# Kernel tuning notes

Measured on AMD Instinct MI355X. Metric: run time of the kernel, lower is better.

The kernel has to match this reference:

```python
import jax, jax.numpy as jnp
import numpy as np

PI = 3.141592653589793


def _nearest_idx(g, size):
    # PyTorch grid_sample nearest, align_corners=False: unnormalize then round half up
    x = ((g + 1.0) * size - 1.0) / 2.0
    return jnp.clip(jnp.floor(x + 0.5).astype(jnp.int32), 0, size - 1)


def setup_inputs() -> dict:
    key = jax.random.key(0)
    ks = jax.random.split(key, 12)
    B, Q, H, W, C, Cf = 1, 65536, 64, 64, 256, 128
    scale = 4  # HR is 256x256
    inp = {
        'inp_img': jax.random.uniform(ks[0], (B, 3, H, W), jnp.float32),
        'coef': jax.random.normal(ks[1], (B, C, H, W), jnp.float32) * 0.5,
        'freq': jax.random.normal(ks[2], (B, Cf, H, W), jnp.float32) * 0.5,
        'coord': jax.random.uniform(ks[3], (B, Q, 2), jnp.float32, minval=-1.0, maxval=1.0),
        'cell': jnp.full((B, Q, 2), 2.0 / (H * scale), jnp.float32),
        'w_coord_fc': jax.random.normal(ks[4], (128, 2), jnp.float32) * 0.5,
        'w_phase': jax.random.normal(ks[5], (128, 2), jnp.float32) * 0.5,
        'w1': jax.random.normal(ks[6], (256, 256), jnp.float32) * (1.0 / 16.0),
        'b1': jnp.zeros((256,), jnp.float32),
        'w2': jax.random.normal(ks[7], (256, 256), jnp.float32) * (1.0 / 16.0),
        'b2': jnp.zeros((256,), jnp.float32),
        'w3': jax.random.normal(ks[8], (3, 256), jnp.float32) * (1.0 / 16.0),
        'b3': jnp.zeros((3,), jnp.float32),
    }
    return inp


def reference(inp_img, coef, freq, coord, cell, w_coord_fc, w_phase, w1, b1, w2, b2, w3, b3):
    B, C, H, W = coef.shape
    Q = coord.shape[1]
    eps = 1e-6
    rx = 1.0 / H  # 2/H/2
    ry = 1.0 / W
    # 4 local-ensemble offsets in loop order (vx,vy) in {-1,1}x{-1,1}
    offs = jnp.array([[-1.0, -1.0], [-1.0, 1.0], [1.0, -1.0], [1.0, 1.0]], jnp.float32)
    shift = offs * jnp.array([rx, ry], jnp.float32) + eps  # [4,2]
    coord_ = jnp.clip(coord[:, None, :, :] + shift[None, :, None, :], -1.0 + eps, 1.0 - eps)  # [B,4,Q,2]

    # coord channel 0 -> H axis, channel 1 -> W axis (after flip(-1) in torch)
    iy = _nearest_idx(coord_[..., 0], H)  # [B,4,Q]
    ix = _nearest_idx(coord_[..., 1], W)
    lin = iy * W + ix  # [B,4,Q]

    def gather(fmap):  # fmap [B,Cc,H,W] -> [B,4,Q,Cc]
        Cc = fmap.shape[1]
        flat = fmap.reshape(B, Cc, H * W).transpose(0, 2, 1)  # [B,HW,Cc]
        return jax.vmap(lambda f, i: f[i])(flat, lin.reshape(B, -1)).reshape(B, 4, Q, Cc)

    q_coef = gather(coef)   # [B,4,Q,256]
    q_freq = gather(freq)   # [B,4,Q,128]

    # feat_coord at nearest pixel = pixel centers from make_coord
    qc_y = -1.0 + (2.0 * iy.astype(jnp.float32) + 1.0) / H
    qc_x = -1.0 + (2.0 * ix.astype(jnp.float32) + 1.0) / W
    rel0 = (coord[:, None, :, 0] - qc_y) * H  # [B,4,Q]
    rel1 = (coord[:, None, :, 1] - qc_x) * W
    rel_coord = jnp.stack([rel0, rel1], axis=-1)  # [B,4,Q,2]
    rel_cell = cell * jnp.array([H, W], jnp.float32)  # [B,Q,2]

    q_freq = q_freq * jnp.einsum('boqd,kd->boqk', rel_coord, w_coord_fc)
    q_freq = q_freq + jnp.einsum('bqd,kd->bqk', rel_cell, w_phase)[:, None]
    q_freq = jnp.concatenate([jnp.cos(PI * q_freq), jnp.sin(PI * q_freq)], axis=-1)  # [B,4,Q,256]

    x = q_coef * q_freq
    h = jax.nn.relu(jnp.einsum('boqc,dc->boqd', x, w1) + b1)
    h = jax.nn.relu(jnp.einsum('boqc,dc->boqd', h, w2) + b2)
    preds = jnp.einsum('boqc,dc->boqd', h, w3) + b3  # [B,4,Q,3]

    area = jnp.abs(rel0 * rel1) + 1e-9  # [B,4,Q]
    tot = jnp.sum(area, axis=1, keepdims=True)
    weights = area[:, ::-1] / tot  # swap 0<->3, 1<->2
    ret = jnp.sum(preds * weights[..., None], axis=1)  # [B,Q,3]

    # bilinear grid_sample of inp_img, padding_mode='border', align_corners=False
    hi, wi = inp_img.shape[-2:]
    gy = jnp.clip(((coord[..., 0] + 1.0) * hi - 1.0) / 2.0, 0.0, hi - 1.0)
    gx = jnp.clip(((coord[..., 1] + 1.0) * wi - 1.0) / 2.0, 0.0, wi - 1.0)
    y0 = jnp.floor(gy).astype(jnp.int32); x0 = jnp.floor(gx).astype(jnp.int32)
    y1 = jnp.clip(y0 + 1, 0, hi - 1); x1 = jnp.clip(x0 + 1, 0, wi - 1)
    wy = gy - y0.astype(jnp.float32); wx = gx - x0.astype(jnp.float32)
    img_flat = inp_img.reshape(B, 3, hi * wi).transpose(0, 2, 1)  # [B,HW,3]
    g = lambda yy, xx: jax.vmap(lambda f, i: f[i])(img_flat, yy * wi + xx)  # [B,Q,3]
    samp = (g(y0, x0) * ((1 - wy) * (1 - wx))[..., None]
            + g(y0, x1) * ((1 - wy) * wx)[..., None]
            + g(y1, x0) * (wy * (1 - wx))[..., None]
            + g(y1, x1) * (wy * wx)[..., None])
    return ret + samp
```

## Files before the change

kernel.cpp:

```cpp
#include <hip/hip_runtime.h>
#include <math.h>

typedef __bf16 bf16_t;
typedef bf16_t bf16x8 __attribute__((ext_vector_type(8)));
typedef bf16_t bf16x4 __attribute__((ext_vector_type(4)));
typedef float  f32x4  __attribute__((ext_vector_type(4)));

constexpr int H = 64, W = 64, Q = 65536;
constexpr int C = 256, CF = 128;
constexpr int QPB = 32;
constexpr int PADC = 264;


__global__ void transpose_cvt_kernel(const float* __restrict__ src, bf16_t* __restrict__ dst, int Crows) {
    __shared__ float tile[32][33];
    int bx = blockIdx.x * 32;
    int by = blockIdx.y * 32;
    int tx = threadIdx.x & 31;
    int ty = threadIdx.x >> 5;
#pragma unroll
    for (int i = 0; i < 4; i++)
        tile[ty + i * 8][tx] = src[(by + ty + i * 8) * 4096 + bx + tx];
    __syncthreads();
#pragma unroll
    for (int i = 0; i < 4; i++)
        dst[(bx + ty + i * 8) * Crows + by + tx] = (bf16_t)tile[tx][ty + i * 8];
}

__global__ void cvt_w_kernel(const float* __restrict__ w1, const float* __restrict__ w2,
                             bf16_t* __restrict__ w1b, bf16_t* __restrict__ w2b) {
    int i = blockIdx.x * 256 + threadIdx.x;
    w1b[i] = (bf16_t)w1[i];
    w2b[i] = (bf16_t)w2[i];
}

__global__ void pack_tab_kernel(const float* __restrict__ wcf, const float* __restrict__ wph,
                                float4* __restrict__ wtab) {
    int k = threadIdx.x;
    float4 v;
    v.x = wcf[k * 2 + 0]; v.y = wcf[k * 2 + 1];
    v.z = wph[k * 2 + 0]; v.w = wph[k * 2 + 1];
    wtab[k] = v;
}

__global__ void cvt_w3_kernel(const float* __restrict__ w3, bf16_t* __restrict__ w3p) {
    int k = threadIdx.x;
#pragma unroll
    for (int n = 0; n < 16; n++)
        w3p[n * 256 + k] = (n < 3) ? (bf16_t)w3[n * 256 + k] : (bf16_t)0.f;
}


#define LOADB(dst, Wptr, kb)                                                                  \
    {                                                                                         \
        dst[0] = *(const bf16x8*)((Wptr) + (wv * 32 + l15) * 256 + (kb) * 32 + l16 * 8);      \
        dst[1] = *(const bf16x8*)((Wptr) + (wv * 32 + 16 + l15) * 256 + (kb) * 32 + l16 * 8); \
    }

__global__ __launch_bounds__(512, 4)
void lte_fused_kernel(const bf16_t* __restrict__ coefT,
                      const bf16_t* __restrict__ freqT,
                      const bf16_t* __restrict__ w1b,
                      const bf16_t* __restrict__ w2b,
                      const bf16_t* __restrict__ w3p,
                      const float4* __restrict__ wtab,
                      const float* __restrict__ img,
                      const float* __restrict__ coord,
                      const float* __restrict__ cell,
                      const float* __restrict__ b1,
                      const float* __restrict__ b2,
                      const float* __restrict__ b3,
                      float* __restrict__ out)
{
    extern __shared__ char smem[];
    bf16_t* buf    = (bf16_t*)smem;
    float*  areaS  = (float*)(smem + 67584);
    float*  predsS = (float*)(smem + 68096);

    const int t    = threadIdx.x;
    const int lane = t & 63;
    const int wv   = t >> 6;
    const int l15  = lane & 15;
    const int l16  = lane >> 4;

    {
        const int row = t >> 2;
        const int t4  = t & 3;
        const int qL  = row >> 2;
        const int o   = row & 3;
        const int q   = blockIdx.x * QPB + qL;
        const float c0  = coord[q * 2 + 0];
        const float c1  = coord[q * 2 + 1];
        const float rc0 = cell[q * 2 + 0] * (float)H;
        const float rc1 = cell[q * 2 + 1] * (float)W;
        const float vx = (o & 2) ? 1.f : -1.f;
        const float vy = (o & 1) ? 1.f : -1.f;
        const float EPS = 1e-6f;
        float g0 = fminf(fmaxf(c0 + vx * (1.f / H) + EPS, -1.f + EPS), 1.f - EPS);
        float g1 = fminf(fmaxf(c1 + vy * (1.f / W) + EPS, -1.f + EPS), 1.f - EPS);
        int iy = (int)floorf(((g0 + 1.f) * (float)H - 1.f) * 0.5f + 0.5f);
        iy = min(max(iy, 0), H - 1);
        int ix = (int)floorf(((g1 + 1.f) * (float)W - 1.f) * 0.5f + 0.5f);
        ix = min(max(ix, 0), W - 1);
        const float rel0 = (c0 - (-1.f + (2.f * (float)iy + 1.f) / (float)H)) * (float)H;
        const float rel1 = (c1 - (-1.f + (2.f * (float)ix + 1.f) / (float)W)) * (float)W;
        if (t4 == 0) areaS[row] = fabsf(rel0 * rel1) + 1e-9f;
        const int pix = iy * W + ix;
        const bf16_t* fq = freqT + pix * CF;
        const bf16_t* cf = coefT + pix * C;
        const int k0 = t4 * 32;

        bf16x8 fqv[4], ccv[4], csv[4];
#pragma unroll
        for (int i = 0; i < 4; i++) {
            fqv[i] = *(const bf16x8*)(fq + k0 + i * 8);
            ccv[i] = *(const bf16x8*)(cf + k0 + i * 8);
            csv[i] = *(const bf16x8*)(cf + 128 + k0 + i * 8);
        }
#pragma unroll
        for (int i = 0; i < 4; i++) {
            bf16x8 vc, vs;
#pragma unroll
            for (int j = 0; j < 8; j++) {
                const int k = k0 + i * 8 + j;
                const float4 tv = wtab[k];
                const float proj = rel0 * tv.x + rel1 * tv.y;
                const float ph   = rc0 * tv.z + rc1 * tv.w;
                const float m = (float)fqv[i][j] * proj + ph;
                const float xr  = __builtin_amdgcn_fractf(m * 0.5f);
                const float s   = __builtin_amdgcn_sinf(xr);
                const float cst = __builtin_amdgcn_cosf(xr);
                vc[j] = (bf16_t)((float)ccv[i][j] * cst);
                vs[j] = (bf16_t)((float)csv[i][j] * s);
            }
            *(bf16x8*)(buf + row * PADC + k0 + i * 8)       = vc;
            *(bf16x8*)(buf + row * PADC + 128 + k0 + i * 8) = vs;
        }
    }

    bf16x8 b1q[8][2];
    LOADB(b1q[0], w1b, 0);
    LOADB(b1q[1], w1b, 1);
    __syncthreads();

    bf16x8 b2q[8][2];
    {
        f32x4 acc[8][2];
#pragma unroll
        for (int mi = 0; mi < 8; mi++)
#pragma unroll
            for (int nf = 0; nf < 2; nf++) {
                f32x4 z = {0.f, 0.f, 0.f, 0.f};
                acc[mi][nf] = z;
            }
#pragma unroll
        for (int kb = 0; kb < 8; kb++) {
            if (kb < 6) { LOADB(b1q[kb + 2], w1b, kb + 2); }
            bf16x8 a[8];
#pragma unroll
            for (int mi = 0; mi < 8; mi++)
                a[mi] = *(bf16x8*)(buf + (mi * 16 + l15) * PADC + kb * 32 + l16 * 8);
#pragma unroll
            for (int mi = 0; mi < 8; mi++)
#pragma unroll
                for (int nf = 0; nf < 2; nf++)
                    acc[mi][nf] = __builtin_amdgcn_mfma_f32_16x16x32_bf16(b1q[kb][nf], a[mi], acc[mi][nf], 0, 0, 0);
        }
        LOADB(b2q[0], w2b, 0);
        LOADB(b2q[1], w2b, 1);
        __syncthreads();
#pragma unroll
        for (int nf = 0; nf < 2; nf++) {
            const int colb = wv * 32 + nf * 16 + l16 * 4;
            const float4 bv = *(const float4*)(b1 + colb);
#pragma unroll
            for (int mi = 0; mi < 8; mi++) {
                const int row = mi * 16 + l15;
                bf16x4 h;
                h[0] = (bf16_t)fmaxf(acc[mi][nf][0] + bv.x, 0.f);
                h[1] = (bf16_t)fmaxf(acc[mi][nf][1] + bv.y, 0.f);
                h[2] = (bf16_t)fmaxf(acc[mi][nf][2] + bv.z, 0.f);
                h[3] = (bf16_t)fmaxf(acc[mi][nf][3] + bv.w, 0.f);
                *(bf16x4*)(buf + row * PADC + colb) = h;
            }
        }
        __syncthreads();
    }

    {
        f32x4 acc[8][2];
#pragma unroll
        for (int mi = 0; mi < 8; mi++)
#pragma unroll
            for (int nf = 0; nf < 2; nf++) {
                f32x4 z = {0.f, 0.f, 0.f, 0.f};
                acc[mi][nf] = z;
            }
#pragma unroll
        for (int kb = 0; kb < 8; kb++) {
            if (kb < 6) { LOADB(b2q[kb + 2], w2b, kb + 2); }
            bf16x8 a[8];
#pragma unroll
            for (int mi = 0; mi < 8; mi++)
                a[mi] = *(bf16x8*)(buf + (mi * 16 + l15) * PADC + kb * 32 + l16 * 8);
#pragma unroll
            for (int mi = 0; mi < 8; mi++)
#pragma unroll
                for (int nf = 0; nf < 2; nf++)
                    acc[mi][nf] = __builtin_amdgcn_mfma_f32_16x16x32_bf16(b2q[kb][nf], a[mi], acc[mi][nf], 0, 0, 0);
        }
        __syncthreads();
#pragma unroll
        for (int nf = 0; nf < 2; nf++) {
            const int colb = wv * 32 + nf * 16 + l16 * 4;
            const float4 bv = *(const float4*)(b2 + colb);
#pragma unroll
            for (int mi = 0; mi < 8; mi++) {
                const int row = mi * 16 + l15;
                bf16x4 h;
                h[0] = (bf16_t)fmaxf(acc[mi][nf][0] + bv.x, 0.f);
                h[1] = (bf16_t)fmaxf(acc[mi][nf][1] + bv.y, 0.f);
                h[2] = (bf16_t)fmaxf(acc[mi][nf][2] + bv.z, 0.f);
                h[3] = (bf16_t)fmaxf(acc[mi][nf][3] + bv.w, 0.f);
                *(bf16x4*)(buf + row * PADC + colb) = h;
            }
        }
        __syncthreads();
    }

    {
        f32x4 acc3 = {0.f, 0.f, 0.f, 0.f};
#pragma unroll
        for (int kb = 0; kb < 8; kb++) {
            bf16x8 a = *(bf16x8*)(buf + (wv * 16 + l15) * PADC + kb * 32 + l16 * 8);
            bf16x8 b = *(const bf16x8*)(w3p + l15 * 256 + kb * 32 + l16 * 8);
            acc3 = __builtin_amdgcn_mfma_f32_16x16x32_bf16(a, b, acc3, 0, 0, 0);
        }
        if (l15 < 3) {
            const float bv = b3[l15];
#pragma unroll
            for (int r = 0; r < 4; r++) {
                const int row = wv * 16 + l16 * 4 + r;
                predsS[row * 3 + l15] = acc3[r] + bv;
            }
        }
    }
    __syncthreads();

    if (t < QPB) {
        const int qL = t;
        const int q  = blockIdx.x * QPB + qL;
        const int r0 = qL * 4;
        const float a0 = areaS[r0 + 0], a1 = areaS[r0 + 1], a2 = areaS[r0 + 2], a3 = areaS[r0 + 3];
        const float inv = 1.f / (a0 + a1 + a2 + a3);
        const float wgt0 = a3 * inv, wgt1 = a2 * inv, wgt2 = a1 * inv, wgt3 = a0 * inv;
        const float c0 = coord[q * 2 + 0];
        const float c1 = coord[q * 2 + 1];
        float gy = fminf(fmaxf(((c0 + 1.f) * (float)H - 1.f) * 0.5f, 0.f), (float)(H - 1));
        float gx = fminf(fmaxf(((c1 + 1.f) * (float)W - 1.f) * 0.5f, 0.f), (float)(W - 1));
        int y0 = (int)floorf(gy); int x0 = (int)floorf(gx);
        int y1 = min(y0 + 1, H - 1); int x1 = min(x0 + 1, W - 1);
        const float wy = gy - (float)y0, wx = gx - (float)x0;
#pragma unroll
        for (int ch = 0; ch < 3; ch++) {
            const float ret = predsS[(r0 + 0) * 3 + ch] * wgt0 + predsS[(r0 + 1) * 3 + ch] * wgt1
                            + predsS[(r0 + 2) * 3 + ch] * wgt2 + predsS[(r0 + 3) * 3 + ch] * wgt3;
            const float* ip = img + ch * 4096;
            const float v00 = ip[y0 * 64 + x0], v01 = ip[y0 * 64 + x1];
            const float v10 = ip[y1 * 64 + x0], v11 = ip[y1 * 64 + x1];
            const float samp = v00 * (1.f - wy) * (1.f - wx) + v01 * (1.f - wy) * wx
                             + v10 * wy * (1.f - wx) + v11 * wy * wx;
            out[q * 3 + ch] = ret + samp;
        }
    }
}


extern "C" void kernel_launch(void* const* d_in, const int* in_sizes, int n_in,
                              void* d_out, int out_size, void* d_ws, size_t ws_size,
                              hipStream_t stream) {
    const float* img   = (const float*)d_in[0];
    const float* coef  = (const float*)d_in[1];
    const float* freq  = (const float*)d_in[2];
    const float* coord = (const float*)d_in[3];
    const float* cell  = (const float*)d_in[4];
    const float* wcf   = (const float*)d_in[5];
    const float* wph   = (const float*)d_in[6];
    const float* w1    = (const float*)d_in[7];
    const float* b1    = (const float*)d_in[8];
    const float* w2    = (const float*)d_in[9];
    const float* b2    = (const float*)d_in[10];
    const float* w3    = (const float*)d_in[11];
    const float* b3    = (const float*)d_in[12];
    float* out = (float*)d_out;

    char* ws = (char*)d_ws;
    bf16_t* coefT = (bf16_t*)ws;
    bf16_t* freqT = (bf16_t*)(ws + 2097152);
    bf16_t* w1b   = (bf16_t*)(ws + 3145728);
    bf16_t* w2b   = (bf16_t*)(ws + 3276800);
    float4* wtab  = (float4*)(ws + 3407872);
    bf16_t* w3p   = (bf16_t*)(ws + 3409920);

    transpose_cvt_kernel<<<dim3(128, 8), 256, 0, stream>>>(coef, coefT, 256);
    transpose_cvt_kernel<<<dim3(128, 4), 256, 0, stream>>>(freq, freqT, 128);
    cvt_w_kernel<<<256, 256, 0, stream>>>(w1, w2, w1b, w2b);
    pack_tab_kernel<<<1, 128, 0, stream>>>(wcf, wph, wtab);
    cvt_w3_kernel<<<1, 256, 0, stream>>>(w3, w3p);

    const size_t ldsBytes = 69632;
    lte_fused_kernel<<<Q / QPB, 512, ldsBytes, stream>>>(
        coefT, freqT, w1b, w2b, w3p, wtab, img, coord, cell, b1, b2, b3, out);
}
```

Baseline: 171.8 us.

## Fuse final 256->3 layer into layer-2 epilogue with shuffles and LDS atomics

The third linear layer is now computed straight from layer-2 accumulators in registers. Each lane takes a dot product with fp32 w3 held in registers, the partial sums are reduced across lanes with shuffles, and the per-wave partials are combined in LDS with atomicAdd. This removes the bf16 write-back of h2 to LDS, two barriers, the padded MFMA for 3 outputs and the separate w3 conversion kernel. The final blend is split over 96 threads, one per query and channel, and __syncthreads is replaced by a raw lgkmcnt wait plus s_barrier. The cost is LDS atomic contention, more registers, and a summation order that differs from before.

```diff
diff --git a/kernel.cpp b/kernel.cpp
--- a/kernel.cpp
+++ b/kernel.cpp
@@ -10,6 +10,8 @@
 constexpr int C = 256, CF = 128;
 constexpr int QPB = 32;
 constexpr int PADC = 264;
+
+#define BAR() asm volatile("s_waitcnt lgkmcnt(0)\n\ts_barrier" ::: "memory")
 
 
 __global__ void transpose_cvt_kernel(const float* __restrict__ src, bf16_t* __restrict__ dst, int Crows) {
@@ -43,13 +45,6 @@
     wtab[k] = v;
 }
 
-__global__ void cvt_w3_kernel(const float* __restrict__ w3, bf16_t* __restrict__ w3p) {
-    int k = threadIdx.x;
-#pragma unroll
-    for (int n = 0; n < 16; n++)
-        w3p[n * 256 + k] = (n < 3) ? (bf16_t)w3[n * 256 + k] : (bf16_t)0.f;
-}
-
 
 #define LOADB(dst, Wptr, kb)                                                                  \
     {                                                                                         \
@@ -62,13 +57,13 @@
                       const bf16_t* __restrict__ freqT,
                       const bf16_t* __restrict__ w1b,
                       const bf16_t* __restrict__ w2b,
-                      const bf16_t* __restrict__ w3p,
                       const float4* __restrict__ wtab,
                       const float* __restrict__ img,
                       const float* __restrict__ coord,
                       const float* __restrict__ cell,
                       const float* __restrict__ b1,
                       const float* __restrict__ b2,
+                      const float* __restrict__ w3,
                       const float* __restrict__ b3,
                       float* __restrict__ out)
 {
@@ -82,6 +77,18 @@
     const int wv   = t >> 6;
     const int l15  = lane & 15;
     const int l16  = lane >> 4;
+
+    f32x4 b2r[2], w3r[3][2];
+#pragma unroll
+    for (int nf = 0; nf < 2; nf++) {
+        const int colb = wv * 32 + nf * 16 + l16 * 4;
+        b2r[nf] = *(const f32x4*)(b2 + colb);
+#pragma unroll
+        for (int ch = 0; ch < 3; ch++)
+            w3r[ch][nf] = *(const f32x4*)(w3 + ch * 256 + colb);
+    }
+
+    if (t < 384) predsS[t] = 0.f;
 
     {
         const int row = t >> 2;
@@ -141,7 +148,7 @@
     bf16x8 b1q[8][2];
     LOADB(b1q[0], w1b, 0);
     LOADB(b1q[1], w1b, 1);
-    __syncthreads();
+    BAR();
 
     bf16x8 b2q[8][2];
     {
@@ -168,7 +175,7 @@
         }
         LOADB(b2q[0], w2b, 0);
         LOADB(b2q[1], w2b, 1);
-        __syncthreads();
+        BAR();
 #pragma unroll
         for (int nf = 0; nf < 2; nf++) {
             const int colb = wv * 32 + nf * 16 + l16 * 4;
@@ -184,7 +191,7 @@
                 *(bf16x4*)(buf + row * PADC + colb) = h;
             }
         }
-        __syncthreads();
+        BAR();
     }
 
     {
@@ -209,51 +216,42 @@
                 for (int nf = 0; nf < 2; nf++)
                     acc[mi][nf] = __builtin_amdgcn_mfma_f32_16x16x32_bf16(b2q[kb][nf], a[mi], acc[mi][nf], 0, 0, 0);
         }
-        __syncthreads();
-#pragma unroll
-        for (int nf = 0; nf < 2; nf++) {
-            const int colb = wv * 32 + nf * 16 + l16 * 4;
-            const float4 bv = *(const float4*)(b2 + colb);
-#pragma unroll
-            for (int mi = 0; mi < 8; mi++) {
-                const int row = mi * 16 + l15;
-                bf16x4 h;
-                h[0] = (bf16_t)fmaxf(acc[mi][nf][0] + bv.x, 0.f);
-                h[1] = (bf16_t)fmaxf(acc[mi][nf][1] + bv.y, 0.f);
-                h[2] = (bf16_t)fmaxf(acc[mi][nf][2] + bv.z, 0.f);
-                h[3] = (bf16_t)fmaxf(acc[mi][nf][3] + bv.w, 0.f);
-                *(bf16x4*)(buf + row * PADC + colb) = h;
-            }
-        }
-        __syncthreads();
-    }
-
-    {
-        f32x4 acc3 = {0.f, 0.f, 0.f, 0.f};
-#pragma unroll
-        for (int kb = 0; kb < 8; kb++) {
-            bf16x8 a = *(bf16x8*)(buf + (wv * 16 + l15) * PADC + kb * 32 + l16 * 8);
-            bf16x8 b = *(const bf16x8*)(w3p + l15 * 256 + kb * 32 + l16 * 8);
-            acc3 = __builtin_amdgcn_mfma_f32_16x16x32_bf16(a, b, acc3, 0, 0, 0);
-        }
-        if (l15 < 3) {
-            const float bv = b3[l15];
-#pragma unroll
-            for (int r = 0; r < 4; r++) {
-                const int row = wv * 16 + l16 * 4 + r;
-                predsS[row * 3 + l15] = acc3[r] + bv;
-            }
-        }
-    }
-    __syncthreads();
-
-    if (t < QPB) {
-        const int qL = t;
+#pragma unroll
+        for (int mi = 0; mi < 8; mi++) {
+            float h2v[2][4];
+#pragma unroll
+            for (int nf = 0; nf < 2; nf++)
+#pragma unroll
+                for (int r = 0; r < 4; r++)
+                    h2v[nf][r] = fmaxf(acc[mi][nf][r] + b2r[nf][r], 0.f);
+#pragma unroll
+            for (int ch = 0; ch < 3; ch++) {
+                float p = 0.f;
+#pragma unroll
+                for (int nf = 0; nf < 2; nf++)
+#pragma unroll
+                    for (int r = 0; r < 4; r++)
+                        p = fmaf(h2v[nf][r], w3r[ch][nf][r], p);
+                p += __shfl_xor(p, 16);
+                p += __shfl_xor(p, 32);
+                if (l16 == 0)
+                    atomicAdd(&predsS[(mi * 16 + l15) * 3 + ch], p);
+            }
+        }
+    }
+    BAR();
+
+    if (t < 96) {
+        const int ch = t >> 5;
+        const int qL = t & 31;
         const int q  = blockIdx.x * QPB + qL;
         const int r0 = qL * 4;
         const float a0 = areaS[r0 + 0], a1 = areaS[r0 + 1], a2 = areaS[r0 + 2], a3 = areaS[r0 + 3];
         const float inv = 1.f / (a0 + a1 + a2 + a3);
         const float wgt0 = a3 * inv, wgt1 = a2 * inv, wgt2 = a1 * inv, wgt3 = a0 * inv;
+        const float ret = predsS[(r0 + 0) * 3 + ch] * wgt0 + predsS[(r0 + 1) * 3 + ch] * wgt1
+                        + predsS[(r0 + 2) * 3 + ch] * wgt2 + predsS[(r0 + 3) * 3 + ch] * wgt3
+                        + b3[ch];
         const float c0 = coord[q * 2 + 0];
         const float c1 = coord[q * 2 + 1];
         float gy = fminf(fmaxf(((c0 + 1.f) * (float)H - 1.f) * 0.5f, 0.f), (float)(H - 1));
@@ -261,17 +259,12 @@
         int y0 = (int)floorf(gy); int x0 = (int)floorf(gx);
         int y1 = min(y0 + 1, H - 1); int x1 = min(x0 + 1, W - 1);
         const float wy = gy - (float)y0, wx = gx - (float)x0;
-#pragma unroll
-        for (int ch = 0; ch < 3; ch++) {
-            const float ret = predsS[(r0 + 0) * 3 + ch] * wgt0 + predsS[(r0 + 1) * 3 + ch] * wgt1
-                            + predsS[(r0 + 2) * 3 + ch] * wgt2 + predsS[(r0 + 3) * 3 + ch] * wgt3;
-            const float* ip = img + ch * 4096;
-            const float v00 = ip[y0 * 64 + x0], v01 = ip[y0 * 64 + x1];
-            const float v10 = ip[y1 * 64 + x0], v11 = ip[y1 * 64 + x1];
-            const float samp = v00 * (1.f - wy) * (1.f - wx) + v01 * (1.f - wy) * wx
-                             + v10 * wy * (1.f - wx) + v11 * wy * wx;
-            out[q * 3 + ch] = ret + samp;
-        }
+        const float* ip = img + ch * 4096;
+        const float v00 = ip[y0 * 64 + x0], v01 = ip[y0 * 64 + x1];
+        const float v10 = ip[y1 * 64 + x0], v11 = ip[y1 * 64 + x1];
+        const float samp = v00 * (1.f - wy) * (1.f - wx) + v01 * (1.f - wy) * wx
+                         + v10 * wy * (1.f - wx) + v11 * wy * wx;
+        out[q * 3 + ch] = ret + samp;
     }
 }
 
@@ -300,15 +293,13 @@
     bf16_t* w1b   = (bf16_t*)(ws + 3145728);
     bf16_t* w2b   = (bf16_t*)(ws + 3276800);
     float4* wtab  = (float4*)(ws + 3407872);
-    bf16_t* w3p   = (bf16_t*)(ws + 3409920);
 
     transpose_cvt_kernel<<<dim3(128, 8), 256, 0, stream>>>(coef, coefT, 256);
     transpose_cvt_kernel<<<dim3(128, 4), 256, 0, stream>>>(freq, freqT, 128);
     cvt_w_kernel<<<256, 256, 0, stream>>>(w1, w2, w1b, w2b);
     pack_tab_kernel<<<1, 128, 0, stream>>>(wcf, wph, wtab);
-    cvt_w3_kernel<<<1, 256, 0, stream>>>(w3, w3p);
 
     const size_t ldsBytes = 69632;
     lte_fused_kernel<<<Q / QPB, 512, ldsBytes, stream>>>(
-        coefT, freqT, w1b, w2b, w3p, wtab, img, coord, cell, b1, b2, b3, out);
-}
+        coefT, freqT, w1b, w2b, wtab, img, coord, cell, b1, b2, w3, b3, out);
+}
```

Measured after the change: 207.8 us. 1.21x slower.
